# Kernel tuning notes

Measured on AMD Instinct MI355X. Metric: run time of the kernel, lower is better.

## Reference

```python
import jax, jax.numpy as jnp
import numpy as np

B, S, D, H = 4, 2048, 768, 12
HD = D // H
SCALE = HD ** -0.5


def setup_inputs() -> dict:
    key = jax.random.key(0)
    ks = jax.random.split(key, 10)
    inp = {
        "x": jax.random.normal(ks[0], (B, S, D), jnp.float32),
        "attn_mask": jax.random.normal(ks[1], (B, S), jnp.float32),
        "Wq": jax.random.normal(ks[2], (D, D), jnp.float32) * (D ** -0.5),
        "bq": jax.random.normal(ks[3], (D,), jnp.float32) * 0.02,
        "Wk": jax.random.normal(ks[4], (D, D), jnp.float32) * (D ** -0.5),
        "bk": jax.random.normal(ks[5], (D,), jnp.float32) * 0.02,
        "Wv": jax.random.normal(ks[6], (D, D), jnp.float32) * (D ** -0.5),
        "bv": jax.random.normal(ks[7], (D,), jnp.float32) * 0.02,
        "Wo": jax.random.normal(ks[8], (D, D), jnp.float32) * (D ** -0.5),
        "bo": jax.random.normal(ks[9], (D,), jnp.float32) * 0.02,
    }
    return inp


def _split_heads(e):
    # [B, S, D] -> [B, H, S, HD]
    return e.reshape(B, S, H, HD).transpose(0, 2, 1, 3)


def reference(x, attn_mask, Wq, bq, Wk, bk, Wv, bv, Wo, bo):
    q = _split_heads((x @ Wq + bq) * SCALE)          # [B,H,S,HD]
    k = _split_heads(x @ Wk + bk)                     # [B,H,S,HD]
    v = _split_heads(x @ Wv + bv)                     # [B,H,S,HD]
    scores = jnp.einsum('bhsd,bhtd->bhst', q, k)      # [B,H,S,S]
    scores = scores + attn_mask[:, None, None, :]     # additive mask over keys
    probs = jax.nn.softmax(scores, axis=-1)
    out = jnp.einsum('bhst,bhtd->bhsd', probs, v)     # [B,H,S,HD]
    out = out.transpose(0, 2, 1, 3).reshape(B, S, D)  # merge heads
    return out @ Wo + bo
```

## Files before the change

kernel.cpp:

```cpp
#include <hip/hip_runtime.h>
#include <cmath>

#define B_ 4
#define S_ 2048
#define D_ 768
#define H_ 12
#define HD_ 64
#define SCALE_ 0.125f
#define LOG2E_ 1.4426950408889634f
#define M_ 8192

typedef unsigned short ushortT;
typedef __attribute__((ext_vector_type(8))) __bf16 bf16x8;
typedef __attribute__((ext_vector_type(4))) __bf16 bf16x4;
typedef __attribute__((ext_vector_type(4))) float f32x4;
typedef __attribute__((ext_vector_type(4))) short s16x4;

typedef __attribute__((address_space(1))) const void glb_cv;
typedef __attribute__((address_space(3))) void lds_v;

__device__ inline ushortT f2bf(float f) {
    return __builtin_bit_cast(ushortT, (__bf16)f);
}

__device__ inline void gload_lds16(const void* g, void* l) {
    __builtin_amdgcn_global_load_lds((glb_cv*)g, (lds_v*)l, 16, 0, 0);
}

__device__ inline f32x4 mfma16(bf16x4 a, bf16x4 b, f32x4 c) {
#if __has_builtin(__builtin_amdgcn_mfma_f32_16x16x16_bf16)
    return __builtin_amdgcn_mfma_f32_16x16x16_bf16(a, b, c, 0, 0, 0);
#elif __has_builtin(__builtin_amdgcn_mfma_f32_16x16x16bf16_1k)
    return __builtin_amdgcn_mfma_f32_16x16x16bf16_1k(
        __builtin_bit_cast(s16x4, a), __builtin_bit_cast(s16x4, b), c, 0, 0, 0);
#else
    asm("v_mfma_f32_16x16x16_bf16 %0, %1, %2, %0" : "+v"(c) : "v"(a), "v"(b));
    return c;
#endif
}

__global__ __launch_bounds__(256)
void convert_f32_bf16(const float* __restrict__ in, ushortT* __restrict__ out)
{
    const size_t i = ((size_t)blockIdx.x * 256 + threadIdx.x) * 8;
    float4 a = *(const float4*)(in + i);
    float4 b = *(const float4*)(in + i + 4);
    union { ushortT u[8]; float4 f; } o;
    o.u[0] = f2bf(a.x); o.u[1] = f2bf(a.y); o.u[2] = f2bf(a.z); o.u[3] = f2bf(a.w);
    o.u[4] = f2bf(b.x); o.u[5] = f2bf(b.y); o.u[6] = f2bf(b.z); o.u[7] = f2bf(b.w);
    *(float4*)(out + i) = o.f;
}

__global__ __launch_bounds__(256)
void transpose_w(const float* __restrict__ W0, const float* __restrict__ W1,
                 const float* __restrict__ W2, const float* __restrict__ W3,
                 ushortT* __restrict__ wt4)
{
    const float* W = (blockIdx.z == 0) ? W0 : (blockIdx.z == 1) ? W1
                   : (blockIdx.z == 2) ? W2 : W3;
    ushortT* o = wt4 + (size_t)blockIdx.z * 768 * 768;
    __shared__ float T[64][65];
    const int tid = threadIdx.x;
    const int k0 = blockIdx.x * 64, n0 = blockIdx.y * 64;

    for (int t = tid; t < 1024; t += 256) {
        const int r = t >> 4, c4 = (t & 15) << 2;
        float4 v = *(const float4*)&W[(size_t)(k0 + r) * 768 + n0 + c4];
        T[r][c4 + 0] = v.x; T[r][c4 + 1] = v.y;
        T[r][c4 + 2] = v.z; T[r][c4 + 3] = v.w;
    }
    __syncthreads();
    for (int t = tid; t < 1024; t += 256) {
        const int r = t >> 4, c4 = (t & 15) << 2;
        union { ushortT u[4]; unsigned long long v; } ov;
        ov.u[0] = f2bf(T[c4 + 0][r]); ov.u[1] = f2bf(T[c4 + 1][r]);
        ov.u[2] = f2bf(T[c4 + 2][r]); ov.u[3] = f2bf(T[c4 + 3][r]);
        *(unsigned long long*)&o[(size_t)(n0 + r) * 768 + k0 + c4] = ov.v;
    }
}

__device__ inline void gemm_core_128x64(
    const ushortT* __restrict__ A, const ushortT* __restrict__ Bt,
    ushortT* As, ushortT* Bs, int m0, int n0, f32x4 acc[4][2])
{
    const int tid  = threadIdx.x;
    const int lane = tid & 63;
    const int wave = tid >> 6;
    const int lr = lane & 15, lg = lane >> 4;
    const int wr = wave >> 1, wc = wave & 1;

    #pragma unroll
    for (int mi = 0; mi < 4; ++mi)
        #pragma unroll
        for (int ni = 0; ni < 2; ++ni)
            acc[mi][ni] = (f32x4){0.f, 0.f, 0.f, 0.f};

    #pragma unroll 1
    for (int k0 = 0; k0 < 768; k0 += 64) {
        __syncthreads();
        #pragma unroll
        for (int it = 0; it < 4; ++it) {
            const int ci = it * 256 + tid;
            const int row = ci >> 3, c = ci & 7;
            const int sc = c ^ (row & 7);
            gload_lds16(A + (size_t)(m0 + row) * 768 + k0 + sc * 8,
                        As + (size_t)(it * 256 + wave * 64) * 8);
        }
        #pragma unroll
        for (int it = 0; it < 2; ++it) {
            const int ci = it * 256 + tid;
            const int row = ci >> 3, c = ci & 7;
            const int sc = c ^ (row & 7);
            gload_lds16(Bt + (size_t)(n0 + row) * 768 + k0 + sc * 8,
                        Bs + (size_t)(it * 256 + wave * 64) * 8);
        }
        __syncthreads();

        #pragma unroll
        for (int ks = 0; ks < 2; ++ks) {
            bf16x8 af[4], bfr[2];
            #pragma unroll
            for (int mi = 0; mi < 4; ++mi) {
                const int row = wr * 64 + mi * 16 + lr;
                const int ch = (ks * 4 + lg) ^ (row & 7);
                af[mi] = __builtin_bit_cast(bf16x8, *(const float4*)(As + row * 64 + ch * 8));
            }
            #pragma unroll
            for (int ni = 0; ni < 2; ++ni) {
                const int row = wc * 32 + ni * 16 + lr;
                const int ch = (ks * 4 + lg) ^ (row & 7);
                bfr[ni] = __builtin_bit_cast(bf16x8, *(const float4*)(Bs + row * 64 + ch * 8));
            }
            #pragma unroll
            for (int mi = 0; mi < 4; ++mi)
                #pragma unroll
                for (int ni = 0; ni < 2; ++ni)
                    acc[mi][ni] = __builtin_amdgcn_mfma_f32_16x16x32_bf16(
                        af[mi], bfr[ni], acc[mi][ni], 0, 0, 0);
        }
    }
}

__global__ __launch_bounds__(256)
void qkv_gemm(const ushortT* __restrict__ xb, const ushortT* __restrict__ wt4,
              const float* __restrict__ bq, const float* __restrict__ bk,
              const float* __restrict__ bv,
              ushortT* __restrict__ qb, ushortT* __restrict__ kb,
              ushortT* __restrict__ vtb)
{
    __shared__ __align__(16) ushortT As[128 * 64];
    __shared__ __align__(16) ushortT Bs[64 * 64];
    const int z = blockIdx.z;
    const ushortT* Wt = wt4 + (size_t)z * 768 * 768;
    const float* bias = (z == 0) ? bq : (z == 1) ? bk : bv;
    const float scale = (z == 0) ? (SCALE_ * LOG2E_) : 1.0f;

    const int m0 = blockIdx.x * 128, n0 = blockIdx.y * 64;
    f32x4 acc[4][2];
    gemm_core_128x64(xb, Wt, As, Bs, m0, n0, acc);

    const int tid = threadIdx.x;
    const int lane = tid & 63, wave = tid >> 6;
    const int lr = lane & 15, lg = lane >> 4;
    const int wr = wave >> 1, wc = wave & 1;
    const int h = n0 >> 6;

    if (z == 2) {
        #pragma unroll
        for (int ni = 0; ni < 2; ++ni) {
            const int nn = wc * 32 + ni * 16 + lr;
            const float bb = bias[n0 + nn];
            #pragma unroll
            for (int mi = 0; mi < 4; ++mi) {
                const int mb = m0 + wr * 64 + mi * 16 + lg * 4;
                const int b = mb >> 11, s = mb & 2047;
                ushort4 ov;
                ov.x = f2bf(acc[mi][ni][0] + bb);
                ov.y = f2bf(acc[mi][ni][1] + bb);
                ov.z = f2bf(acc[mi][ni][2] + bb);
                ov.w = f2bf(acc[mi][ni][3] + bb);
                *(ushort4*)&vtb[(((size_t)b * H_ + h) * HD_ + nn) * S_ + s] = ov;
            }
        }
    } else {
        ushortT* out = (z == 0) ? qb : kb;
        #pragma unroll
        for (int ni = 0; ni < 2; ++ni) {
            const int nn = wc * 32 + ni * 16 + lr;
            const float bb = bias[n0 + nn];
            #pragma unroll
            for (int mi = 0; mi < 4; ++mi) {
                #pragma unroll
                for (int j = 0; j < 4; ++j) {
                    const int m = m0 + wr * 64 + mi * 16 + lg * 4 + j;
                    const int b = m >> 11, s = m & 2047;
                    out[(((size_t)b * H_ + h) * S_ + s) * HD_ + nn] =
                        f2bf((acc[mi][ni][j] + bb) * scale);
                }
            }
        }
    }
}

__global__ __launch_bounds__(256)
void o_gemm(const ushortT* __restrict__ ab, const ushortT* __restrict__ wto,
            const float* __restrict__ bo, float* __restrict__ out)
{
    __shared__ __align__(16) ushortT As[128 * 64];
    __shared__ __align__(16) ushortT Bs[64 * 64];
    const int m0 = blockIdx.x * 128, n0 = blockIdx.y * 64;
    f32x4 acc[4][2];
    gemm_core_128x64(ab, wto, As, Bs, m0, n0, acc);

    const int tid = threadIdx.x;
    const int lane = tid & 63, wave = tid >> 6;
    const int lr = lane & 15, lg = lane >> 4;
    const int wr = wave >> 1, wc = wave & 1;

    #pragma unroll
    for (int ni = 0; ni < 2; ++ni) {
        const int n = n0 + wc * 32 + ni * 16 + lr;
        const float bb = bo[n];
        #pragma unroll
        for (int mi = 0; mi < 4; ++mi) {
            #pragma unroll
            for (int j = 0; j < 4; ++j) {
                const int m = m0 + wr * 64 + mi * 16 + lg * 4 + j;
                out[(size_t)m * 768 + n] = acc[mi][ni][j] + bb;
            }
        }
    }
}

__global__ __launch_bounds__(128, 2)
void attn_mfma(const ushortT* __restrict__ Q, const ushortT* __restrict__ K,
               const ushortT* __restrict__ Vt, const float* __restrict__ mask,
               ushortT* __restrict__ out)
{
    __shared__ __align__(16) ushortT Ks[2][64 * 64];
    __shared__ __align__(16) ushortT Vs[2][64 * 64];
    __shared__ float Ms[S_];

    const int tid  = threadIdx.x;
    const int lane = tid & 63;
    const int wave = tid >> 6;
    const int lr   = lane & 15;
    const int lg   = lane >> 4;

    const int gid  = blockIdx.x;
    const int xcd  = gid & 7;
    const int w    = gid >> 3;
    const int bh_i = xcd * 6 + (w >> 4);
    const int q0   = (w & 15) * 128;
    const int b    = bh_i / H_;
    const int h    = bh_i % H_;
    const size_t bh = (size_t)bh_i;

    for (int f = tid; f < 512; f += 128) {
        float4 mv = *(const float4*)&mask[(size_t)b * S_ + f * 4];
        mv.x *= LOG2E_; mv.y *= LOG2E_; mv.z *= LOG2E_; mv.w *= LOG2E_;
        *(float4*)&Ms[f * 4] = mv;
    }

    bf16x8 qf[4][2];
    #pragma unroll
    for (int g = 0; g < 4; ++g) {
        const ushortT* Qg = Q + (bh * S_ + q0 + wave * 64 + g * 16 + lr) * HD_;
        qf[g][0] = __builtin_bit_cast(bf16x8, *(const float4*)(Qg + lg * 8));
        qf[g][1] = __builtin_bit_cast(bf16x8, *(const float4*)(Qg + 32 + lg * 8));
    }

    const ushortT* Kg = K  + bh * S_ * HD_;
    const ushortT* Vg = Vt + bh * HD_ * S_;

    bf16x4 onesA;
    #pragma unroll
    for (int i = 0; i < 4; ++i) onesA[i] = (__bf16)1.0f;

    f32x4 acc[4][4];
    f32x4 accl[4];
    #pragma unroll
    for (int g = 0; g < 4; ++g) {
        #pragma unroll
        for (int cb = 0; cb < 4; ++cb) acc[g][cb] = (f32x4){0.f, 0.f, 0.f, 0.f};
        accl[g] = (f32x4){0.f, 0.f, 0.f, 0.f};
    }

    auto stage = [&](int bsel, int k0) {
        #pragma unroll
        for (int it = 0; it < 4; ++it) {
            const int ci = it * 128 + tid;
            const int row = ci >> 3, c = ci & 7, sc = c ^ (row & 7);
            gload_lds16(Kg + (size_t)(k0 + row) * HD_ + sc * 8,
                        &Ks[bsel][(it * 128 + wave * 64) * 8]);
        }
        #pragma unroll
        for (int it = 0; it < 4; ++it) {
            const int ci = it * 128 + tid;
            const int row = ci >> 3, c = ci & 7, sc = c ^ (row & 7);
            gload_lds16(Vg + (size_t)row * S_ + k0 + sc * 8,
                        &Vs[bsel][(it * 128 + wave * 64) * 8]);
        }
    };

    stage(0, 0);
    __syncthreads();

    for (int kt = 0; kt < S_ / 64; ++kt) {
        const int k0 = kt * 64;
        const int buf = kt & 1;
        if (kt + 1 < S_ / 64) stage(buf ^ 1, k0 + 64);

        bf16x8 kf[4][2];
        #pragma unroll
        for (int cb = 0; cb < 4; ++cb) {
            #pragma unroll
            for (int ks = 0; ks < 2; ++ks) {
                const int rk = cb * 16 + lr;
                const int pp = (ks * 4 + lg) ^ (rk & 7);
                kf[cb][ks] = __builtin_bit_cast(bf16x8,
                    *(const float4*)(&Ks[buf][rk * 64 + pp * 8]));
            }
        }
        f32x4 mv[4];
        #pragma unroll
        for (int cb = 0; cb < 4; ++cb)
            mv[cb] = __builtin_bit_cast(f32x4,
                *(const float4*)&Ms[k0 + cb * 16 + lg * 4]);

        bf16x4 vf[4][4];
        #pragma unroll
        for (int cbh = 0; cbh < 4; ++cbh) {
            const int rv = cbh * 16 + lr;
            #pragma unroll
            for (int sl = 0; sl < 4; ++sl) {
                const int cg = sl * 2 + (lg >> 1);
                const int cl = cg ^ (rv & 7);
                vf[cbh][sl] = __builtin_bit_cast(bf16x4,
                    *(const ulonglong1*)(&Vs[buf][rv * 64 + cl * 8 + (lg & 1) * 4]));
            }
        }

        #pragma unroll
        for (int g = 0; g < 4; ++g) {
            f32x4 s[4];
            __builtin_amdgcn_s_setprio(1);
            #pragma unroll
            for (int cb = 0; cb < 4; ++cb) {
                s[cb] = __builtin_amdgcn_mfma_f32_16x16x32_bf16(
                    kf[cb][0], qf[g][0], mv[cb], 0, 0, 0);
                s[cb] = __builtin_amdgcn_mfma_f32_16x16x32_bf16(
                    kf[cb][1], qf[g][1], s[cb], 0, 0, 0);
            }
            __builtin_amdgcn_s_setprio(0);

            bf16x4 pb[4];
            #pragma unroll
            for (int cb = 0; cb < 4; ++cb) {
                pb[cb][0] = (__bf16)exp2f(s[cb][0]);
                pb[cb][1] = (__bf16)exp2f(s[cb][1]);
                pb[cb][2] = (__bf16)exp2f(s[cb][2]);
                pb[cb][3] = (__bf16)exp2f(s[cb][3]);
            }

            __builtin_amdgcn_s_setprio(1);
            #pragma unroll
            for (int sl = 0; sl < 4; ++sl) {
                #pragma unroll
                for (int cbh = 0; cbh < 4; ++cbh)
                    acc[g][cbh] = mfma16(vf[cbh][sl], pb[sl], acc[g][cbh]);
                accl[g] = mfma16(onesA, pb[sl], accl[g]);
            }
            __builtin_amdgcn_s_setprio(0);
        }

        __syncthreads();
    }

    asm volatile("s_nop 7\n\ts_nop 7" ::: );

    #pragma unroll
    for (int g = 0; g < 4; ++g) {
        const float inv = 1.f / accl[g][0];
        const size_t row = (size_t)b * S_ + q0 + wave * 64 + g * 16 + lr;
        #pragma unroll
        for (int cbh = 0; cbh < 4; ++cbh) {
            ushort4 ov;
            ov.x = f2bf(acc[g][cbh][0] * inv);
            ov.y = f2bf(acc[g][cbh][1] * inv);
            ov.z = f2bf(acc[g][cbh][2] * inv);
            ov.w = f2bf(acc[g][cbh][3] * inv);
            *(ushort4*)&out[row * D_ + h * HD_ + cbh * 16 + lg * 4] = ov;
        }
    }
}

extern "C" void kernel_launch(void* const* d_in, const int* in_sizes, int n_in,
                              void* d_out, int out_size, void* d_ws, size_t ws_size,
                              hipStream_t stream)
{
    const float* x    = (const float*)d_in[0];
    const float* mask = (const float*)d_in[1];
    const float* Wq   = (const float*)d_in[2];
    const float* bq   = (const float*)d_in[3];
    const float* Wk   = (const float*)d_in[4];
    const float* bk   = (const float*)d_in[5];
    const float* Wv   = (const float*)d_in[6];
    const float* bv   = (const float*)d_in[7];
    const float* Wo   = (const float*)d_in[8];
    const float* bo   = (const float*)d_in[9];
    float* out = (float*)d_out;

    const size_t NE = (size_t)B_ * S_ * D_;
    ushortT* xb  = (ushortT*)d_ws;
    ushortT* qb  = xb + NE;
    ushortT* kb  = qb + NE;
    ushortT* vtb = kb + NE;
    ushortT* ab  = vtb + NE;
    ushortT* wt4 = ab + NE;

    convert_f32_bf16<<<NE / 2048, 256, 0, stream>>>(x, xb);
    transpose_w<<<dim3(12, 12, 4), 256, 0, stream>>>(Wq, Wk, Wv, Wo, wt4);

    qkv_gemm<<<dim3(M_ / 128, 12, 3), 256, 0, stream>>>(
        xb, wt4, bq, bk, bv, qb, kb, vtb);

    attn_mfma<<<768, 128, 0, stream>>>(qb, kb, vtb, mask, ab);

    o_gemm<<<dim3(M_ / 128, 12), 256, 0, stream>>>(
        ab, wt4 + 3 * 768 * 768, bo, out);
}
```

Measured before the change: 187.2 us.

## Switch attention to 32x32x16 MFMA tiles with permlane-swapped probabilities and VALU row sums

Rewrites the attention inner loop to use 32x32x16 bf16 MFMAs for both QK^T and PV instead of 16x16 tiles. The probabilities are repacked in registers with v_permlane32_swap, so the transposed P layout comes without LDS traffic. The row-sum MFMA against a ones vector is replaced by a VALU sum of the bf16-rounded probabilities. The log2e-scaled mask moves into a separate small kernel, so the mask is read from global memory instead of LDS, and stage addresses become precomputed incrementing pointers. This cuts MFMA instruction count and LDS use. The cost is more VALU work, higher register pressure from the 16-wide accumulators, and an extra kernel launch.

```diff
diff --git a/kernel.cpp b/kernel.cpp
--- a/kernel.cpp
+++ b/kernel.cpp
@@ -11,10 +11,10 @@
 #define M_ 8192
 
 typedef unsigned short ushortT;
+typedef unsigned int u32;
 typedef __attribute__((ext_vector_type(8))) __bf16 bf16x8;
-typedef __attribute__((ext_vector_type(4))) __bf16 bf16x4;
 typedef __attribute__((ext_vector_type(4))) float f32x4;
-typedef __attribute__((ext_vector_type(4))) short s16x4;
+typedef __attribute__((ext_vector_type(16))) float f32x16;
 
 typedef __attribute__((address_space(1))) const void glb_cv;
 typedef __attribute__((address_space(3))) void lds_v;
@@ -23,20 +23,18 @@
     return __builtin_bit_cast(ushortT, (__bf16)f);
 }
 
+__device__ inline u32 pk2bf(float a, float b) {
+    return (u32)__builtin_bit_cast(ushortT, (__bf16)a)
+         | ((u32)__builtin_bit_cast(ushortT, (__bf16)b) << 16);
+}
+
+__device__ inline float sum2bf(u32 u) {
+    return __builtin_bit_cast(float, u << 16)
+         + __builtin_bit_cast(float, u & 0xffff0000u);
+}
+
 __device__ inline void gload_lds16(const void* g, void* l) {
     __builtin_amdgcn_global_load_lds((glb_cv*)g, (lds_v*)l, 16, 0, 0);
-}
-
-__device__ inline f32x4 mfma16(bf16x4 a, bf16x4 b, f32x4 c) {
-#if __has_builtin(__builtin_amdgcn_mfma_f32_16x16x16_bf16)
-    return __builtin_amdgcn_mfma_f32_16x16x16_bf16(a, b, c, 0, 0, 0);
-#elif __has_builtin(__builtin_amdgcn_mfma_f32_16x16x16bf16_1k)
-    return __builtin_amdgcn_mfma_f32_16x16x16bf16_1k(
-        __builtin_bit_cast(s16x4, a), __builtin_bit_cast(s16x4, b), c, 0, 0, 0);
-#else
-    asm("v_mfma_f32_16x16x16_bf16 %0, %1, %2, %0" : "+v"(c) : "v"(a), "v"(b));
-    return c;
-#endif
 }
 
 __global__ __launch_bounds__(256)
@@ -49,6 +47,13 @@
     o.u[0] = f2bf(a.x); o.u[1] = f2bf(a.y); o.u[2] = f2bf(a.z); o.u[3] = f2bf(a.w);
     o.u[4] = f2bf(b.x); o.u[5] = f2bf(b.y); o.u[6] = f2bf(b.z); o.u[7] = f2bf(b.w);
     *(float4*)(out + i) = o.f;
+}
+
+__global__ __launch_bounds__(256)
+void scale_mask(const float* __restrict__ in, float* __restrict__ outp)
+{
+    const int i = blockIdx.x * 256 + threadIdx.x;
+    outp[i] = in[i] * LOG2E_;
 }
 
 __global__ __launch_bounds__(256)
@@ -234,18 +239,17 @@
 
 __global__ __launch_bounds__(128, 2)
 void attn_mfma(const ushortT* __restrict__ Q, const ushortT* __restrict__ K,
-               const ushortT* __restrict__ Vt, const float* __restrict__ mask,
+               const ushortT* __restrict__ Vt, const float* __restrict__ msc,
                ushortT* __restrict__ out)
 {
     __shared__ __align__(16) ushortT Ks[2][64 * 64];
     __shared__ __align__(16) ushortT Vs[2][64 * 64];
-    __shared__ float Ms[S_];
 
     const int tid  = threadIdx.x;
     const int lane = tid & 63;
-    const int wave = tid >> 6;
-    const int lr   = lane & 15;
-    const int lg   = lane >> 4;
+    const int wq   = tid >> 6;
+    const int col  = lane & 31;
+    const int hi   = lane >> 5;
 
     const int gid  = blockIdx.x;
     const int xcd  = gid & 7;
@@ -256,141 +260,170 @@
     const int h    = bh_i % H_;
     const size_t bh = (size_t)bh_i;
 
-    for (int f = tid; f < 512; f += 128) {
-        float4 mv = *(const float4*)&mask[(size_t)b * S_ + f * 4];
-        mv.x *= LOG2E_; mv.y *= LOG2E_; mv.z *= LOG2E_; mv.w *= LOG2E_;
-        *(float4*)&Ms[f * 4] = mv;
-    }
-
-    bf16x8 qf[4][2];
-    #pragma unroll
-    for (int g = 0; g < 4; ++g) {
-        const ushortT* Qg = Q + (bh * S_ + q0 + wave * 64 + g * 16 + lr) * HD_;
-        qf[g][0] = __builtin_bit_cast(bf16x8, *(const float4*)(Qg + lg * 8));
-        qf[g][1] = __builtin_bit_cast(bf16x8, *(const float4*)(Qg + 32 + lg * 8));
+    bf16x8 qf[2][4];
+    #pragma unroll
+    for (int qb2 = 0; qb2 < 2; ++qb2) {
+        const ushortT* Qg = Q + (bh * S_ + q0 + wq * 64 + qb2 * 32 + col) * HD_;
+        #pragma unroll
+        for (int ks = 0; ks < 4; ++ks)
+            qf[qb2][ks] = __builtin_bit_cast(bf16x8,
+                *(const float4*)(Qg + ks * 16 + hi * 8));
     }
 
     const ushortT* Kg = K  + bh * S_ * HD_;
     const ushortT* Vg = Vt + bh * HD_ * S_;
-
-    bf16x4 onesA;
-    #pragma unroll
-    for (int i = 0; i < 4; ++i) onesA[i] = (__bf16)1.0f;
-
-    f32x4 acc[4][4];
-    f32x4 accl[4];
-    #pragma unroll
-    for (int g = 0; g < 4; ++g) {
-        #pragma unroll
-        for (int cb = 0; cb < 4; ++cb) acc[g][cb] = (f32x4){0.f, 0.f, 0.f, 0.f};
-        accl[g] = (f32x4){0.f, 0.f, 0.f, 0.f};
-    }
-
-    auto stage = [&](int bsel, int k0) {
+    const float*   mg = msc + (size_t)b * S_;
+
+    const ushortT* ksrc[4];
+    const ushortT* vsrc[4];
+    #pragma unroll
+    for (int it = 0; it < 4; ++it) {
+        const int ci = it * 128 + tid;
+        const int row = ci >> 3, c = ci & 7, sc = c ^ (row & 7);
+        ksrc[it] = Kg + (size_t)row * HD_ + sc * 8;
+        vsrc[it] = Vg + (size_t)row * S_ + sc * 8;
+    }
+
+    int ko[2][4], vo[2][4];
+    #pragma unroll
+    for (int kb2 = 0; kb2 < 2; ++kb2) {
+        const int r = kb2 * 32 + col;
+        #pragma unroll
+        for (int ks = 0; ks < 4; ++ks)
+            ko[kb2][ks] = r * 128 + (((2 * ks + hi) ^ (r & 7)) << 4);
+    }
+    #pragma unroll
+    for (int hb = 0; hb < 2; ++hb) {
+        const int r = hb * 32 + col;
+        #pragma unroll
+        for (int sg = 0; sg < 4; ++sg)
+            vo[hb][sg] = r * 128 + (((2 * sg + hi) ^ (r & 7)) << 4);
+    }
+
+    f32x16 acc[2][2];
+    float accl[2] = {0.f, 0.f};
+    #pragma unroll
+    for (int qb2 = 0; qb2 < 2; ++qb2)
+        #pragma unroll
+        for (int hb = 0; hb < 2; ++hb)
+            #pragma unroll
+            for (int r = 0; r < 16; ++r) acc[qb2][hb][r] = 0.f;
+
+    auto stage = [&](int bsel) {
         #pragma unroll
         for (int it = 0; it < 4; ++it) {
-            const int ci = it * 128 + tid;
-            const int row = ci >> 3, c = ci & 7, sc = c ^ (row & 7);
-            gload_lds16(Kg + (size_t)(k0 + row) * HD_ + sc * 8,
-                        &Ks[bsel][(it * 128 + wave * 64) * 8]);
+            gload_lds16(ksrc[it], &Ks[bsel][(it * 128 + wq * 64) * 8]);
+            ksrc[it] += 64 * HD_;
         }
         #pragma unroll
         for (int it = 0; it < 4; ++it) {
-            const int ci = it * 128 + tid;
-            const int row = ci >> 3, c = ci & 7, sc = c ^ (row & 7);
-            gload_lds16(Vg + (size_t)row * S_ + k0 + sc * 8,
-                        &Vs[bsel][(it * 128 + wave * 64) * 8]);
+            gload_lds16(vsrc[it], &Vs[bsel][(it * 128 + wq * 64) * 8]);
+            vsrc[it] += 64;
         }
     };
 
-    stage(0, 0);
+    stage(0);
     __syncthreads();
 
     for (int kt = 0; kt < S_ / 64; ++kt) {
-        const int k0 = kt * 64;
         const int buf = kt & 1;
-        if (kt + 1 < S_ / 64) stage(buf ^ 1, k0 + 64);
-
-        bf16x8 kf[4][2];
-        #pragma unroll
-        for (int cb = 0; cb < 4; ++cb) {
-            #pragma unroll
-            for (int ks = 0; ks < 2; ++ks) {
-                const int rk = cb * 16 + lr;
-                const int pp = (ks * 4 + lg) ^ (rk & 7);
-                kf[cb][ks] = __builtin_bit_cast(bf16x8,
-                    *(const float4*)(&Ks[buf][rk * 64 + pp * 8]));
-            }
-        }
-        f32x4 mv[4];
-        #pragma unroll
-        for (int cb = 0; cb < 4; ++cb)
-            mv[cb] = __builtin_bit_cast(f32x4,
-                *(const float4*)&Ms[k0 + cb * 16 + lg * 4]);
-
-        bf16x4 vf[4][4];
-        #pragma unroll
-        for (int cbh = 0; cbh < 4; ++cbh) {
-            const int rv = cbh * 16 + lr;
-            #pragma unroll
-            for (int sl = 0; sl < 4; ++sl) {
-                const int cg = sl * 2 + (lg >> 1);
-                const int cl = cg ^ (rv & 7);
-                vf[cbh][sl] = __builtin_bit_cast(bf16x4,
-                    *(const ulonglong1*)(&Vs[buf][rv * 64 + cl * 8 + (lg & 1) * 4]));
-            }
-        }
-
-        #pragma unroll
-        for (int g = 0; g < 4; ++g) {
-            f32x4 s[4];
+        if (kt + 1 < S_ / 64) stage(buf ^ 1);
+
+        f32x16 cin[2];
+        #pragma unroll
+        for (int kb2 = 0; kb2 < 2; ++kb2) {
+            #pragma unroll
+            for (int g = 0; g < 4; ++g) {
+                float4 mv = *(const float4*)(mg + kt * 64 + kb2 * 32 + g * 8 + hi * 4);
+                cin[kb2][4 * g + 0] = mv.x;
+                cin[kb2][4 * g + 1] = mv.y;
+                cin[kb2][4 * g + 2] = mv.z;
+                cin[kb2][4 * g + 3] = mv.w;
+            }
+        }
+
+        bf16x8 kf[2][4];
+        #pragma unroll
+        for (int kb2 = 0; kb2 < 2; ++kb2)
+            #pragma unroll
+            for (int ks = 0; ks < 4; ++ks)
+                kf[kb2][ks] = __builtin_bit_cast(bf16x8,
+                    *(const float4*)((const char*)&Ks[buf][0] + ko[kb2][ks]));
+
+        bf16x8 vf[2][4];
+        #pragma unroll
+        for (int hb = 0; hb < 2; ++hb)
+            #pragma unroll
+            for (int sg = 0; sg < 4; ++sg)
+                vf[hb][sg] = __builtin_bit_cast(bf16x8,
+                    *(const float4*)((const char*)&Vs[buf][0] + vo[hb][sg]));
+
+        #pragma unroll
+        for (int qb2 = 0; qb2 < 2; ++qb2) {
+            u32 bw[4][4];
+            float lsum = 0.f;
+            #pragma unroll
+            for (int kb2 = 0; kb2 < 2; ++kb2) {
+                f32x16 s = cin[kb2];
+                __builtin_amdgcn_s_setprio(1);
+                #pragma unroll
+                for (int ks = 0; ks < 4; ++ks)
+                    s = __builtin_amdgcn_mfma_f32_32x32x16_bf16(
+                        kf[kb2][ks], qf[qb2][ks], s, 0, 0, 0);
+                __builtin_amdgcn_s_setprio(0);
+
+                float p[16];
+                #pragma unroll
+                for (int r = 0; r < 16; ++r) p[r] = exp2f(s[r]);
+
+                #pragma unroll
+                for (int sl = 0; sl < 2; ++sl) {
+                    u32 u0 = pk2bf(p[8 * sl + 0], p[8 * sl + 1]);
+                    u32 u1 = pk2bf(p[8 * sl + 2], p[8 * sl + 3]);
+                    u32 v0 = pk2bf(p[8 * sl + 4], p[8 * sl + 5]);
+                    u32 v1 = pk2bf(p[8 * sl + 6], p[8 * sl + 7]);
+                    lsum += (sum2bf(u0) + sum2bf(u1)) + (sum2bf(v0) + sum2bf(v1));
+                    asm("v_permlane32_swap_b32 %0, %1" : "+v"(u0), "+v"(v0));
+                    asm("v_permlane32_swap_b32 %0, %1" : "+v"(u1), "+v"(v1));
+                    const int sg = kb2 * 2 + sl;
+                    bw[sg][0] = u0; bw[sg][1] = u1;
+                    bw[sg][2] = v0; bw[sg][3] = v1;
+                }
+            }
+            accl[qb2] += lsum + __shfl_xor(lsum, 32);
+
             __builtin_amdgcn_s_setprio(1);
             #pragma unroll
-            for (int cb = 0; cb < 4; ++cb) {
-                s[cb] = __builtin_amdgcn_mfma_f32_16x16x32_bf16(
-                    kf[cb][0], qf[g][0], mv[cb], 0, 0, 0);
-                s[cb] = __builtin_amdgcn_mfma_f32_16x16x32_bf16(
-                    kf[cb][1], qf[g][1], s[cb], 0, 0, 0);
+            for (int sg = 0; sg < 4; ++sg) {
+                union { u32 w[4]; bf16x8 v; } pb;
+                pb.w[0] = bw[sg][0]; pb.w[1] = bw[sg][1];
+                pb.w[2] = bw[sg][2]; pb.w[3] = bw[sg][3];
+                #pragma unroll
+                for (int hb = 0; hb < 2; ++hb)
+                    acc[qb2][hb] = __builtin_amdgcn_mfma_f32_32x32x16_bf16(
+                        vf[hb][sg], pb.v, acc[qb2][hb], 0, 0, 0);
             }
             __builtin_amdgcn_s_setprio(0);
-
-            bf16x4 pb[4];
-            #pragma unroll
-            for (int cb = 0; cb < 4; ++cb) {
-                pb[cb][0] = (__bf16)exp2f(s[cb][0]);
-                pb[cb][1] = (__bf16)exp2f(s[cb][1]);
-                pb[cb][2] = (__bf16)exp2f(s[cb][2]);
-                pb[cb][3] = (__bf16)exp2f(s[cb][3]);
-            }
-
-            __builtin_amdgcn_s_setprio(1);
-            #pragma unroll
-            for (int sl = 0; sl < 4; ++sl) {
-                #pragma unroll
-                for (int cbh = 0; cbh < 4; ++cbh)
-                    acc[g][cbh] = mfma16(vf[cbh][sl], pb[sl], acc[g][cbh]);
-                accl[g] = mfma16(onesA, pb[sl], accl[g]);
-            }
-            __builtin_amdgcn_s_setprio(0);
         }
 
         __syncthreads();
     }
 
-    asm volatile("s_nop 7\n\ts_nop 7" ::: );
-
-    #pragma unroll
-    for (int g = 0; g < 4; ++g) {
-        const float inv = 1.f / accl[g][0];
-        const size_t row = (size_t)b * S_ + q0 + wave * 64 + g * 16 + lr;
-        #pragma unroll
-        for (int cbh = 0; cbh < 4; ++cbh) {
-            ushort4 ov;
-            ov.x = f2bf(acc[g][cbh][0] * inv);
-            ov.y = f2bf(acc[g][cbh][1] * inv);
-            ov.z = f2bf(acc[g][cbh][2] * inv);
-            ov.w = f2bf(acc[g][cbh][3] * inv);
-            *(ushort4*)&out[row * D_ + h * HD_ + cbh * 16 + lg * 4] = ov;
+    #pragma unroll
+    for (int qb2 = 0; qb2 < 2; ++qb2) {
+        const float inv = 1.f / accl[qb2];
+        const size_t row = (size_t)b * S_ + q0 + wq * 64 + qb2 * 32 + col;
+        #pragma unroll
+        for (int hb = 0; hb < 2; ++hb) {
+            #pragma unroll
+            for (int t = 0; t < 4; ++t) {
+                ushort4 ov;
+                ov.x = f2bf(acc[qb2][hb][4 * t + 0] * inv);
+                ov.y = f2bf(acc[qb2][hb][4 * t + 1] * inv);
+                ov.z = f2bf(acc[qb2][hb][4 * t + 2] * inv);
+                ov.w = f2bf(acc[qb2][hb][4 * t + 3] * inv);
+                *(ushort4*)&out[row * D_ + h * HD_ + hb * 32 + t * 8 + hi * 4] = ov;
+            }
         }
     }
 }
@@ -418,15 +451,17 @@
     ushortT* vtb = kb + NE;
     ushortT* ab  = vtb + NE;
     ushortT* wt4 = ab + NE;
+    float*   msc = (float*)(wt4 + (size_t)4 * 768 * 768);
 
     convert_f32_bf16<<<NE / 2048, 256, 0, stream>>>(x, xb);
+    scale_mask<<<(B_ * S_) / 256, 256, 0, stream>>>(mask, msc);
     transpose_w<<<dim3(12, 12, 4), 256, 0, stream>>>(Wq, Wk, Wv, Wo, wt4);
 
     qkv_gemm<<<dim3(M_ / 128, 12, 3), 256, 0, stream>>>(
         xb, wt4, bq, bk, bv, qb, kb, vtb);
 
-    attn_mfma<<<768, 128, 0, stream>>>(qb, kb, vtb, mask, ab);
+    attn_mfma<<<768, 128, 0, stream>>>(qb, kb, vtb, msc, ab);
 
     o_gemm<<<dim3(M_ / 128, 12), 256, 0, stream>>>(
-        ab, wt4 + 3 * 768 * 768, bo, out);
-}
+        ab, wt4 + (size_t)3 * 768 * 768, bo, out);
+}
```

Result: slower. 210.0 us (+12.2%).
